# Performance work log

Hardware: AMD Instinct MI355X
Metric: run time of the kernel (lower is better)

The kernel has to match this reference:

```python
import jax, jax.numpy as jnp
import numpy as np

B, NPG, DIN, ED, DEG = 16, 1024, 16, 8, 32
HEADS, OUT1 = 5, 6
HID = HEADS * OUT1          # 30 features after conv1
C1, C2 = 32, 4              # DIFFPool cluster counts
N = B * NPG                 # 16384 total nodes
E = N * DEG                 # 524288 edges


def _egat_conv(x, src, dst, eattr, W, a_s, a_d, We, heads, outc, n_nodes):
    # Edge-gated GAT: per-edge attention logits from src/dst node features plus
    # a linear projection of edge attributes, segment-softmax over incoming edges.
    h = (x @ W).reshape(n_nodes, heads, outc)
    logit = jax.nn.leaky_relu((h[src] * a_s).sum(-1) + (h[dst] * a_d).sum(-1) + eattr @ We, 0.2)  # [E, heads]
    m = jax.ops.segment_max(logit, dst, num_segments=n_nodes)
    ex = jnp.exp(logit - m[dst])
    den = jax.ops.segment_sum(ex, dst, num_segments=n_nodes)
    alpha = ex / (den[dst] + 1e-16)
    out = jax.ops.segment_sum(alpha[:, :, None] * h[src], dst, num_segments=n_nodes)
    return out.reshape(n_nodes, heads * outc), alpha


def _diff_pool(x, adj, s_logits, b, n, c, d):
    s = jax.nn.softmax(s_logits.reshape(b, n, c), axis=-1)
    xp = jnp.einsum('bnc,bnd->bcd', s, x.reshape(b, n, d))
    adjp = jnp.einsum('bnc,bnm,bmk->bck', s, adj, s)
    reg = jnp.mean((adj - jnp.einsum('bnc,bmc->bnm', s, s)) ** 2)  # link-pred loss
    return xp.reshape(b * c, d), adjp, reg


def _dense_edges(b, c):
    base = jnp.arange(c)
    off = (jnp.arange(b) * c)[:, None]
    src = (jnp.repeat(base, c)[None, :] + off).reshape(-1)
    dst = (jnp.tile(base, c)[None, :] + off).reshape(-1)
    return src, dst


def _forward(x, edge_index, edge_attr, adj, params):
    (W1, a_src1, a_dst1, We1, Wp1, as_p1, ad_p1, Wep1,
     Wp2, as_p2, ad_p2, Wep2, Wf1, bf1, Wf2, bf2) = params
    src, dst = edge_index[0], edge_index[1]
    x1, e = _egat_conv(x, src, dst, edge_attr, W1, a_src1, a_dst1, We1, HEADS, OUT1, N)  # [N,30]
    e_dot = jnp.prod(e, axis=-1)[:, None]  # _EGATConv.dot: product over heads (unused downstream)
    s1, _ = _egat_conv(x1, src, dst, edge_attr, Wp1, as_p1, ad_p1, Wep1, 1, C1, N)
    x2, adj2, reg1 = _diff_pool(x1, adj, s1, B, NPG, C1, HID)
    src2, dst2 = _dense_edges(B, C1)
    ea2 = adj2.reshape(B * C1 * C1, 1)  # pooled graph is dense; adj values as edge attrs
    s2, _ = _egat_conv(x2, src2, dst2, ea2, Wp2, as_p2, ad_p2, Wep2, 1, C2, B * C1)
    x3, _, reg2 = _diff_pool(x2, adj2, s2, B, C1, C2, HID)
    reg = reg1 * 10.0 + reg2 * 0.1
    z = x3.reshape(B, C2 * HID)
    z = jax.nn.relu(z @ Wf1 + bf1)
    logits = z @ Wf2 + bf2
    return logits, reg


def setup_inputs() -> dict:
    key = jax.random.key(0)
    ks = jax.random.split(key, 20)
    # block-diagonal random edges: each graph has NPG*DEG edges within its block
    src_l = jax.random.randint(ks[0], (B, NPG * DEG), 0, NPG)
    dst_l = jax.random.randint(ks[1], (B, NPG * DEG), 0, NPG)
    off = (jnp.arange(B) * NPG)[:, None]
    edge_index = jnp.stack([(src_l + off).reshape(-1), (dst_l + off).reshape(-1)])
    adj = jnp.zeros((B, NPG, NPG), jnp.float32).at[jnp.arange(B)[:, None], src_l, dst_l].set(1.0)
    edge_attr = jax.random.uniform(ks[2], (E, ED), jnp.float32)
    x = jax.random.normal(ks[3], (N, DIN), jnp.float32)
    y = jax.random.randint(ks[4], (B,), 0, 2)

    def nrm(k, shape, fan):
        return jax.random.normal(k, shape, jnp.float32) / np.float32(np.sqrt(fan))

    return dict(
        x=x, edge_index=edge_index, edge_attr=edge_attr, y=y, adj=adj,
        W1=nrm(ks[5], (DIN, HEADS * OUT1), DIN),
        a_src1=nrm(ks[6], (HEADS, OUT1), OUT1),
        a_dst1=nrm(ks[7], (HEADS, OUT1), OUT1),
        We1=nrm(ks[8], (ED, HEADS), ED),
        Wp1=nrm(ks[9], (HID, C1), HID),
        as_p1=nrm(ks[10], (1, C1), C1),
        ad_p1=nrm(ks[11], (1, C1), C1),
        Wep1=nrm(ks[12], (ED, 1), ED),
        Wp2=nrm(ks[13], (HID, C2), HID),
        as_p2=nrm(ks[14], (1, C2), C2),
        ad_p2=nrm(ks[15], (1, C2), C2),
        Wep2=nrm(ks[16], (1, 1), 1),
        Wf1=nrm(ks[17], (C2 * HID, 32), C2 * HID),
        bf1=jnp.zeros((32,), jnp.float32),
        Wf2=nrm(ks[18], (32, 2), 32),
        bf2=jnp.zeros((2,), jnp.float32),
    )


def reference(x, edge_index, edge_attr, y, adj, W1, a_src1, a_dst1, We1, Wp1, as_p1, ad_p1, Wep1, Wp2, as_p2, ad_p2, Wep2, Wf1, bf1, Wf2, bf2):
    params = (W1, a_src1, a_dst1, We1, Wp1, as_p1, ad_p1, Wep1,
              Wp2, as_p2, ad_p2, Wep2, Wf1, bf1, Wf2, bf2)
    return _forward(x, edge_index, edge_attr, adj, params)
```

## Files before the change

kernel.cpp:

```cpp
#include <hip/hip_runtime.h>
#include <math.h>

#define NB 16
#define NPG 1024
#define DIN 16
#define ED 8
#define NHEADS 5
#define OUT1 6
#define HID 30
#define C1 32
#define C2 4
#define NN (NB*NPG)
#define EE (NN*32)
#define EPG 32768
#define CH 16
#define CE 2048

__device__ __forceinline__ float lrelu(float v){ return v >= 0.f ? v : 0.2f*v; }

__device__ __forceinline__ void chunk_gc(int& g, int& c){
    int x = blockIdx.x & 7;
    int j = blockIdx.x >> 3;
    g = x + 8*(j >> 4);
    c = j & 15;
}

__device__ __forceinline__ size_t xcd_chunk_base(){
    int x = blockIdx.x & 7;
    int j = blockIdx.x >> 3;
    int g = x + 8*(j >> 7);
    int c = j & 127;
    return (size_t)g*EPG + (size_t)c*256;
}

__global__ void k_hist_chunk(const int* __restrict__ src, const int* __restrict__ dst,
                             int* __restrict__ histD, int* __restrict__ histS,
                             const float* __restrict__ x, const float* __restrict__ W1,
                             const float* __restrict__ as1, const float* __restrict__ ad1,
                             float* __restrict__ h1, float* __restrict__ hs1, float* __restrict__ hd1){
    int t = threadIdx.x;
    if (blockIdx.x < 256){
        __shared__ int hD[NPG], hS[NPG];
        for (int i = t; i < NPG; i += 256){ hD[i] = 0; hS[i] = 0; }
        __syncthreads();
        int g, c; chunk_gc(g, c);
        size_t e0 = ((size_t)g*CH + c)*CE;
        #pragma unroll
        for (int i = 0; i < 8; i++){
            size_t e = e0 + i*256 + t;
            atomicAdd(&hD[dst[e] & (NPG-1)], 1);
            atomicAdd(&hS[src[e] & (NPG-1)], 1);
        }
        __syncthreads();
        size_t hb = ((size_t)g*CH + c)*NPG;
        for (int i = t; i < NPG; i += 256){
            histD[hb + i] = hD[i];
            histS[hb + i] = hS[i];
        }
        return;
    }
    __shared__ float Ws[DIN*HID];
    __shared__ float as_s[HID], ad_s[HID];
    for (int i = t; i < DIN*HID; i += blockDim.x) Ws[i] = W1[i];
    if (t < HID){ as_s[t] = as1[t]; ad_s[t] = ad1[t]; }
    __syncthreads();
    int n = (blockIdx.x - 256)*blockDim.x + t;
    if (n >= NN) return;
    float xv[DIN];
    #pragma unroll
    for (int i = 0; i < DIN; i++) xv[i] = x[n*DIN + i];
    float hv[HID];
    #pragma unroll
    for (int j = 0; j < HID; j++){
        float a = 0.f;
        #pragma unroll
        for (int i = 0; i < DIN; i++) a += xv[i]*Ws[i*HID + j];
        hv[j] = a; h1[(size_t)n*HID + j] = a;
    }
    #pragma unroll
    for (int h = 0; h < NHEADS; h++){
        float s = 0.f, d = 0.f;
        #pragma unroll
        for (int c2 = 0; c2 < OUT1; c2++){ s += hv[h*OUT1+c2]*as_s[h*OUT1+c2]; d += hv[h*OUT1+c2]*ad_s[h*OUT1+c2]; }
        hs1[n*NHEADS + h] = s; hd1[n*NHEADS + h] = d;
    }
}

__global__ __launch_bounds__(1024) void k_cumscan(int* __restrict__ histD, int* __restrict__ histS,
                                                  int* __restrict__ rowptr, int* __restrict__ rowptrS){
    __shared__ int wtot[16], wbase[16];
    bool isD = (blockIdx.x < NB);
    int b = isD ? blockIdx.x : (blockIdx.x - NB);
    int* hist = isD ? histD : histS;
    int* rp   = isD ? rowptr : rowptrS;
    int n = threadIdx.x;
    int run = 0;
    #pragma unroll
    for (int c = 0; c < CH; c++){
        size_t idx = ((size_t)b*CH + c)*NPG + n;
        int v = hist[idx];
        hist[idx] = run;
        run += v;
    }
    int lane = n & 63, wv = n >> 6;
    int sincl = run;
    #pragma unroll
    for (int off = 1; off < 64; off <<= 1){
        int v = __shfl_up(sincl, off, 64);
        if (lane >= off) sincl += v;
    }
    if (lane == 63) wtot[wv] = sincl;
    __syncthreads();
    if (n == 0){
        int r = 0;
        #pragma unroll
        for (int w = 0; w < 16; w++){ wbase[w] = r; r += wtot[w]; }
    }
    __syncthreads();
    int excl = wbase[wv] + sincl - run;
    rp[b*NPG + n] = b*EPG + excl;
    if (b == NB-1 && n == NPG-1) rp[NN] = EE;
}

__global__ void k_scatter_det(const int* __restrict__ src, const int* __restrict__ dst,
                              const int* __restrict__ rowptr, const int* __restrict__ rowptrS,
                              const int* __restrict__ histD, const int* __restrict__ histS,
                              int* __restrict__ srcs, int* __restrict__ eid,
                              int* __restrict__ dsts, int* __restrict__ nbrS){
    __shared__ int baseD[NPG], baseS[NPG];
    int t = threadIdx.x;
    int g, c; chunk_gc(g, c);
    size_t hb = ((size_t)g*CH + c)*NPG;
    for (int i = t; i < NPG; i += 256){
        baseD[i] = rowptr[g*NPG + i] + histD[hb + i];
        baseS[i] = rowptrS[g*NPG + i] + histS[hb + i];
    }
    __syncthreads();
    size_t e0 = ((size_t)g*CH + c)*CE;
    #pragma unroll
    for (int i = 0; i < 8; i++){
        size_t e = e0 + i*256 + t;
        int s = src[e], d = dst[e];
        int p = atomicAdd(&baseD[d & (NPG-1)], 1);
        srcs[p] = s; eid[p] = (int)e; dsts[p] = d;
        int pS = atomicAdd(&baseS[s & (NPG-1)], 1);
        nbrS[pS] = d;
    }
}

__global__ void k_elogit(const float* __restrict__ ea, const float* __restrict__ We1,
                         const float* __restrict__ Wep1,
                         const int* __restrict__ srcs, const int* __restrict__ eid,
                         const int* __restrict__ dsts,
                         const float* __restrict__ hs1, const float* __restrict__ hd1,
                         float* __restrict__ lg1T, float* __restrict__ ewp1s){
    __shared__ float W[ED*NHEADS];
    __shared__ float Wp[ED];
    int t = threadIdx.x;
    if (t < ED*NHEADS) W[t] = We1[t];
    if (t < ED) Wp[t] = Wep1[t];
    __syncthreads();
    size_t k = xcd_chunk_base() + t;
    int s = srcs[k], e = eid[k], d = dsts[k];
    float a[ED];
    #pragma unroll
    for (int i = 0; i < ED; i++) a[i] = ea[(size_t)e*ED + i];
    const float* hsr = hs1 + (size_t)s*NHEADS;
    const float* hdr = hd1 + (size_t)d*NHEADS;
    #pragma unroll
    for (int h = 0; h < NHEADS; h++){
        float sv = 0.f;
        #pragma unroll
        for (int i = 0; i < ED; i++) sv += a[i]*W[i*NHEADS + h];
        lg1T[(size_t)h*EE + k] = lrelu(hsr[h] + hdr[h] + sv);
    }
    float sv = 0.f;
    #pragma unroll
    for (int i = 0; i < ED; i++) sv += a[i]*Wp[i];
    ewp1s[k] = sv;
}

__global__ __launch_bounds__(640) void k_conv1_agg(const int* __restrict__ srcs,
                            const int* __restrict__ rowptr,
                            const float* __restrict__ h1, const float* __restrict__ lg1T,
                            float* __restrict__ x1){
    __shared__ float hls[NPG*HID];
    int t = threadIdx.x;
    int xx = blockIdx.x & 7;
    int j = blockIdx.x >> 3;
    int g = xx + 8*(j >> 4);
    int seg = j & 15;
    const float* hg = h1 + (size_t)g*NPG*HID;
    for (int i = t; i < NPG*HID; i += 640) hls[i] = hg[i];
    __syncthreads();
    int nl = seg*64 + t/10;
    int r = t - (t/10)*10;
    int h = r >> 1;
    int q = r & 1;
    int n = g*NPG + nl;
    int k0 = rowptr[n], k1 = rowptr[n+1];
    const float* lgh = lg1T + (size_t)h*EE;
    int off = h*OUT1 + q*3;
    float m = -INFINITY, den = 0.f;
    float acc[3] = {0.f, 0.f, 0.f};
    int k = k0;
    for (; k + 4 <= k1; k += 4){
        float l0 = lgh[k+0], l1 = lgh[k+1], l2 = lgh[k+2], l3 = lgh[k+3];
        int s0 = srcs[k+0] & (NPG-1), s1 = srcs[k+1] & (NPG-1);
        int s2 = srcs[k+2] & (NPG-1), s3 = srcs[k+3] & (NPG-1);
        const float* p0 = hls + s0*HID + off;
        const float* p1 = hls + s1*HID + off;
        const float* p2 = hls + s2*HID + off;
        const float* p3 = hls + s3*HID + off;
        float mb = fmaxf(fmaxf(l0, l1), fmaxf(l2, l3));
        float mn = fmaxf(m, mb);
        float f  = expf(m - mn);
        float e0 = expf(l0 - mn), e1 = expf(l1 - mn);
        float e2 = expf(l2 - mn), e3 = expf(l3 - mn);
        m = mn;
        den = den*f + e0 + e1 + e2 + e3;
        #pragma unroll
        for (int c = 0; c < 3; c++)
            acc[c] = acc[c]*f + e0*p0[c] + e1*p1[c] + e2*p2[c] + e3*p3[c];
    }
    for (; k < k1; k++){
        float l = lgh[k];
        int s = srcs[k] & (NPG-1);
        float mn = fmaxf(m, l);
        float f  = expf(m - mn);
        float ex = expf(l - mn);
        m = mn;
        den = den*f + ex;
        const float* hr = hls + s*HID + off;
        #pragma unroll
        for (int c = 0; c < 3; c++) acc[c] = acc[c]*f + ex*hr[c];
    }
    float inv = 1.f / (den + 1e-16f);
    #pragma unroll
    for (int c = 0; c < 3; c++) x1[(size_t)n*HID + off + c] = acc[c]*inv;
}

__global__ void k_pd(const float* __restrict__ x1, const float* __restrict__ Wp1,
                     const float* __restrict__ asp, const float* __restrict__ adp,
                     float* __restrict__ hp1, float* __restrict__ hsp, float* __restrict__ hdp,
                     const int* __restrict__ rowptrS, const int* __restrict__ nbrS,
                     int* __restrict__ unbr, int* __restrict__ ucnt,
                     float* __restrict__ scal){
    __shared__ float Ws[HID*C1];
    __shared__ float as_s[C1], ad_s[C1];
    __shared__ unsigned int bm[256*33];
    __shared__ int red[256];
    int t = threadIdx.x;
    if (blockIdx.x < 64){
        for (int i = t; i < HID*C1; i += blockDim.x) Ws[i] = Wp1[i];
        if (t < C1){ as_s[t] = asp[t]; ad_s[t] = adp[t]; }
        __syncthreads();
        int n = blockIdx.x*blockDim.x + t;
        float xv[HID];
        #pragma unroll
        for (int d = 0; d < HID; d++) xv[d] = x1[(size_t)n*HID + d];
        float s = 0.f, dd = 0.f;
        for (int c = 0; c < C1; c++){
            float a = 0.f;
            #pragma unroll
            for (int d = 0; d < HID; d++) a += xv[d]*Ws[d*C1 + c];
            hp1[(size_t)n*C1 + c] = a;
            s += a*as_s[c]; dd += a*ad_s[c];
        }
        hsp[n] = s; hdp[n] = dd;
        return;
    }
    unsigned int* mybm = &bm[t*33];
    #pragma unroll
    for (int i = 0; i < 32; i++) mybm[i] = 0u;
    int n = (blockIdx.x - 64)*blockDim.x + t;
    int cnt = 0;
    {
        int k0 = rowptrS[n], k1 = rowptrS[n+1];
        for (int k = k0; k < k1; k++){
            int m = nbrS[k];
            int loc = m & (NPG-1);
            unsigned int w = (unsigned int)(loc >> 5);
            unsigned int bit = 1u << (loc & 31);
            unsigned int old = mybm[w];
            if (!(old & bit)){
                mybm[w] = old | bit;
                unbr[k0 + cnt] = m;
                cnt++;
            }
        }
        ucnt[n] = cnt;
    }
    red[t] = cnt; __syncthreads();
    for (int s = 128; s > 0; s >>= 1){ if (t < s) red[t] += red[t+s]; __syncthreads(); }
    if (t == 0) atomicAdd(&scal[0], (float)red[0]);
}

__global__ __launch_bounds__(512) void k_pool1_agg(const int* __restrict__ srcs,
                            const int* __restrict__ rowptr,
                            const float* __restrict__ hp1, const float* __restrict__ hsp,
                            const float* __restrict__ hdp, const float* __restrict__ ewp1s,
                            float* __restrict__ ssoft){
    __shared__ float hls[NPG*33];
    __shared__ float sm[64*33];
    __shared__ float hsps[NPG];
    __shared__ float hdps[64];
    int t = threadIdx.x;
    int xx = blockIdx.x & 7;
    int j = blockIdx.x >> 3;
    int g = xx + 8*(j >> 4);
    int seg = j & 15;
    const float* hg = hp1 + (size_t)g*NPG*C1;
    for (int i = t; i < NPG*C1; i += 512){
        int s = i >> 5, c = i & 31;
        hls[s*33 + c] = hg[i];
    }
    for (int i = t; i < NPG; i += 512) hsps[i] = hsp[g*NPG + i];
    if (t < 64) hdps[t] = hdp[g*NPG + seg*64 + t];
    __syncthreads();
    int nl = t >> 3, q = t & 7;
    int n = g*NPG + seg*64 + nl;
    int k0 = rowptr[n], k1 = rowptr[n+1];
    float hdv = hdps[nl];
    float m = -INFINITY, den = 0.f;
    float acc[4] = {0.f, 0.f, 0.f, 0.f};
    int k = k0;
    for (; k + 4 <= k1; k += 4){
        int sl0 = srcs[k+0] & (NPG-1), sl1 = srcs[k+1] & (NPG-1);
        int sl2 = srcs[k+2] & (NPG-1), sl3 = srcs[k+3] & (NPG-1);
        float l0 = lrelu(hsps[sl0] + hdv + ewp1s[k+0]);
        float l1 = lrelu(hsps[sl1] + hdv + ewp1s[k+1]);
        float l2 = lrelu(hsps[sl2] + hdv + ewp1s[k+2]);
        float l3 = lrelu(hsps[sl3] + hdv + ewp1s[k+3]);
        int b0 = sl0*33 + q*4, b1 = sl1*33 + q*4;
        int b2 = sl2*33 + q*4, b3 = sl3*33 + q*4;
        float mb = fmaxf(fmaxf(l0, l1), fmaxf(l2, l3));
        float mn = fmaxf(m, mb);
        float f  = expf(m - mn);
        float e0 = expf(l0 - mn), e1 = expf(l1 - mn);
        float e2 = expf(l2 - mn), e3 = expf(l3 - mn);
        m = mn;
        den = den*f + e0 + e1 + e2 + e3;
        #pragma unroll
        for (int c = 0; c < 4; c++)
            acc[c] = acc[c]*f + e0*hls[b0+c] + e1*hls[b1+c] + e2*hls[b2+c] + e3*hls[b3+c];
    }
    for (; k < k1; k++){
        int sl = srcs[k] & (NPG-1);
        float l = lrelu(hsps[sl] + hdv + ewp1s[k]);
        int b = sl*33 + q*4;
        float mn = fmaxf(m, l);
        float f  = expf(m - mn);
        float ex = expf(l - mn);
        m = mn;
        den = den*f + ex;
        #pragma unroll
        for (int c = 0; c < 4; c++) acc[c] = acc[c]*f + ex*hls[b+c];
    }
    float inv = 1.f / (den + 1e-16f);
    #pragma unroll
    for (int c = 0; c < 4; c++) sm[nl*33 + q*4 + c] = acc[c]*inv;
    __syncthreads();
    float mx = -INFINITY;
    #pragma unroll 8
    for (int i = 0; i < C1; i++) mx = fmaxf(mx, sm[nl*33 + i]);
    float sum = 0.f;
    #pragma unroll 8
    for (int i = 0; i < C1; i++) sum += expf(sm[nl*33 + i] - mx);
    float is = 1.f/sum;
    #pragma unroll
    for (int c = 0; c < 4; c++)
        ssoft[(size_t)n*C1 + q*4 + c] = expf(sm[nl*33 + q*4 + c] - mx)*is;
}

__global__ __launch_bounds__(512) void k_T(const int* __restrict__ rowptrS,
                    const int* __restrict__ unbr,
                    const int* __restrict__ ucnt, const float* __restrict__ ssoft,
                    float* __restrict__ T){
    __shared__ float sls[NPG*33];
    int t = threadIdx.x;
    int xx = blockIdx.x & 7;
    int j = blockIdx.x >> 3;
    int g = xx + 8*(j >> 4);
    int seg = j & 15;
    const float* sg = ssoft + (size_t)g*NPG*C1;
    for (int i = t; i < NPG*C1; i += 512){
        int s = i >> 5, c = i & 31;
        sls[s*33 + c] = sg[i];
    }
    __syncthreads();
    int nl = t >> 3, q = t & 7;
    int n = g*NPG + seg*64 + nl;
    int k0 = rowptrS[n];
    int cnt = ucnt[n];
    float acc[4] = {0.f, 0.f, 0.f, 0.f};
    int i = 0;
    for (; i + 4 <= cnt; i += 4){
        int b0 = (unbr[k0+i+0] & (NPG-1))*33 + q*4;
        int b1 = (unbr[k0+i+1] & (NPG-1))*33 + q*4;
        int b2 = (unbr[k0+i+2] & (NPG-1))*33 + q*4;
        int b3 = (unbr[k0+i+3] & (NPG-1))*33 + q*4;
        #pragma unroll
        for (int c = 0; c < 4; c++)
            acc[c] += sls[b0+c] + sls[b1+c] + sls[b2+c] + sls[b3+c];
    }
    for (; i < cnt; i++){
        int b = (unbr[k0+i] & (NPG-1))*33 + q*4;
        #pragma unroll
        for (int c = 0; c < 4; c++) acc[c] += sls[b+c];
    }
    #pragma unroll
    for (int c = 0; c < 4; c++) T[(size_t)n*C1 + q*4 + c] = acc[c];
}

__global__ void k_partials(const float* __restrict__ ssoft, const float* __restrict__ T,
                           const float* __restrict__ x1,
                           float* __restrict__ adj2, float* __restrict__ Gm,
                           float* __restrict__ x2){
    int b  = blockIdx.y;
    int n0 = blockIdx.x * 64;
    int t  = threadIdx.x;
    __shared__ float ssh[64*C1];
    __shared__ float tsh[64*C1];
    __shared__ float xsh[64*HID];
    {
        size_t sbase = ((size_t)b*NPG + n0)*C1;
        #pragma unroll
        for (int i = 0; i < 8; i++){
            int lin = t + i*256;
            ssh[lin] = ssoft[sbase + lin];
            tsh[lin] = T[sbase + lin];
        }
        size_t xbase = ((size_t)b*NPG + n0)*HID;
        for (int lin = t; lin < 64*HID; lin += 256) xsh[lin] = x1[xbase + lin];
    }
    __syncthreads();
    float accA[4] = {0,0,0,0}, accG[4] = {0,0,0,0}, accX[4] = {0,0,0,0};
    int cA[4], kA[4], cX[4], dX[4];
    #pragma unroll
    for (int q = 0; q < 4; q++){
        int p = t + q*256;
        cA[q] = p >> 5; kA[q] = p & 31;
        cX[q] = p / HID; dX[q] = p - cX[q]*HID;
    }
    for (int r = 0; r < 64; r++){
        const float* sr = ssh + r*C1;
        const float* tr = tsh + r*C1;
        const float* xr = xsh + r*HID;
        #pragma unroll
        for (int q = 0; q < 4; q++){
            float sc = sr[cA[q]];
            accA[q] += sc*tr[kA[q]];
            accG[q] += sc*sr[kA[q]];
        }
        #pragma unroll
        for (int q = 0; q < 4; q++){
            int p = t + q*256;
            if (p < C1*HID) accX[q] += sr[cX[q]]*xr[dX[q]];
        }
    }
    #pragma unroll
    for (int q = 0; q < 4; q++){
        int p = t + q*256;
        atomicAdd(&adj2[(size_t)b*1024 + p], accA[q]);
        atomicAdd(&Gm[(size_t)b*1024 + p], accG[q]);
        if (p < C1*HID) atomicAdd(&x2[((size_t)b*C1 + cX[q])*HID + dX[q]], accX[q]);
    }
}

__global__ __launch_bounds__(256) void k_tail(const float* __restrict__ x2, const float* __restrict__ adj2,
                       const float* __restrict__ Gm,
                       const float* __restrict__ Wp2, const float* __restrict__ asp,
                       const float* __restrict__ adp, const float* __restrict__ Wep2,
                       const float* __restrict__ Wf1, const float* __restrict__ bf1,
                       const float* __restrict__ Wf2, const float* __restrict__ bf2,
                       float* __restrict__ out, float* __restrict__ scal,
                       unsigned int* __restrict__ ctr){
    int b = blockIdx.x;
    int t = threadIdx.x;
    __shared__ float x2s[C1*HID];
    __shared__ float a2s[C1*C1];
    __shared__ float Wps[HID*C2];
    __shared__ float Wf1s[C2*HID*32];
    __shared__ float asps[C2], adps[C2];
    __shared__ float bf1s[32], Wf2s[64], bf2s[2];
    __shared__ float wepsh;
    __shared__ float h2s[C1*C2];
    __shared__ float hs2s[C1], hd2s[C1];
    __shared__ float sss[C1*C2];
    __shared__ float x3s[C2*HID];
    __shared__ float zsh[32];
    __shared__ float red[256], red2[256];

    float gv[4];
    #pragma unroll
    for (int q = 0; q < 4; q++) gv[q] = Gm[(size_t)b*1024 + t + q*256];
    for (int i = t; i < C1*HID; i += 256) x2s[i] = x2[(size_t)b*C1*HID + i];
    for (int i = t; i < C1*C1; i += 256) a2s[i] = adj2[(size_t)b*C1*C1 + i];
    for (int i = t; i < C2*HID*32; i += 256) Wf1s[i] = Wf1[i];
    if (t < HID*C2) Wps[t] = Wp2[t];
    if (t < C2){ asps[t] = asp[t]; adps[t] = adp[t]; }
    if (t < 32) bf1s[t] = bf1[t];
    if (t < 64) Wf2s[t] = Wf2[t];
    if (t < 2)  bf2s[t] = bf2[t];
    if (t == 0) wepsh = Wep2[0];
    __syncthreads();

    if (t < C1*C2){
        int i = t >> 2, c = t & 3;
        float a = 0.f;
        #pragma unroll
        for (int d = 0; d < HID; d++) a += x2s[i*HID + d]*Wps[d*C2 + c];
        h2s[t] = a;
    }
    {
        float lfr = gv[0]*gv[0] + gv[1]*gv[1] + gv[2]*gv[2] + gv[3]*gv[3];
        float ltr = (t < C1) ? a2s[t*33] : 0.f;
        red[t] = ltr; red2[t] = lfr;
        __syncthreads();
        for (int s = 128; s > 0; s >>= 1){
            if (t < s){ red[t] += red[t+s]; red2[t] += red2[t+s]; }
            __syncthreads();
        }
        if (t == 0){ atomicAdd(&scal[1], red[0]); atomicAdd(&scal[2], red2[0]); }
    }
    if (t < C1){
        float s = 0.f, dd = 0.f;
        #pragma unroll
        for (int c = 0; c < C2; c++){ s += h2s[t*C2 + c]*asps[c]; dd += h2s[t*C2 + c]*adps[c]; }
        hs2s[t] = s; hd2s[t] = dd;
    }
    __syncthreads();
    if (t < C1){
        int j = t;
        float hdv = hd2s[j];
        float wep = wepsh;
        float m = -INFINITY;
        for (int i = 0; i < C1; i++)
            m = fmaxf(m, lrelu(hs2s[i] + hdv + a2s[i*C1 + j]*wep));
        float den = 0.f;
        float acc[C2] = {0,0,0,0};
        for (int i = 0; i < C1; i++){
            float ex = expf(lrelu(hs2s[i] + hdv + a2s[i*C1 + j]*wep) - m);
            den += ex;
            #pragma unroll
            for (int c = 0; c < C2; c++) acc[c] += ex * h2s[i*C2 + c];
        }
        float inv = 1.f/(den + 1e-16f);
        float v[C2]; float mx = -INFINITY;
        #pragma unroll
        for (int c = 0; c < C2; c++){ v[c] = acc[c]*inv; mx = fmaxf(mx, v[c]); }
        float sum = 0.f;
        #pragma unroll
        for (int c = 0; c < C2; c++){ v[c] = expf(v[c] - mx); sum += v[c]; }
        float i2 = 1.f/sum;
        #pragma unroll
        for (int c = 0; c < C2; c++) sss[j*C2 + c] = v[c]*i2;
    }
    __syncthreads();
    if (t < C2*HID){
        int c = t / HID, d = t % HID;
        float a = 0.f;
        #pragma unroll
        for (int n = 0; n < C1; n++) a += sss[n*C2 + c]*x2s[n*HID + d];
        x3s[t] = a;
    }
    {
        float loc = 0.f;
        for (int p = t; p < 1024; p += 256){
            int n = p >> 5, mm = p & 31;
            float dot = 0.f;
            #pragma unroll
            for (int c = 0; c < C2; c++) dot += sss[n*C2 + c]*sss[mm*C2 + c];
            float df = a2s[p] - dot;
            loc += df*df;
        }
        red[t] = loc; __syncthreads();
        for (int s = 128; s > 0; s >>= 1){ if (t < s) red[t] += red[t+s]; __syncthreads(); }
        if (t == 0) atomicAdd(&scal[3], red[0]);
        __syncthreads();
    }
    if (t < 32){
        float a = bf1s[t];
        #pragma unroll 8
        for (int k = 0; k < C2*HID; k++) a += x3s[k]*Wf1s[k*32 + t];
        zsh[t] = fmaxf(a, 0.f);
    }
    __syncthreads();
    if (t < 2){
        float a = bf2s[t];
        #pragma unroll
        for (int j = 0; j < 32; j++) a += zsh[j]*Wf2s[j*2 + t];
        out[b*2 + t] = a;
    }
    if (t == 0){
        __threadfence();
        unsigned int old = atomicAdd(ctr, 1u);
        if (old == NB - 1){
            float adjsum = atomicAdd(&scal[0], 0.f);
            float tr     = atomicAdd(&scal[1], 0.f);
            float fr     = atomicAdd(&scal[2], 0.f);
            float r2     = atomicAdd(&scal[3], 0.f);
            float reg1 = (adjsum - 2.f*tr + fr) * (1.f/16777216.f);
            float reg2 = r2 * (1.f/16384.f);
            out[32] = 10.f*reg1 + 0.1f*reg2;
        }
    }
}

extern "C" void kernel_launch(void* const* d_in, const int* in_sizes, int n_in,
                              void* d_out, int out_size, void* d_ws, size_t ws_size,
                              hipStream_t stream) {
    const float* x    = (const float*)d_in[0];
    const int*   ei   = (const int*)d_in[1];
    const float* ea   = (const float*)d_in[2];
    const float* W1   = (const float*)d_in[5];
    const float* as1  = (const float*)d_in[6];
    const float* ad1  = (const float*)d_in[7];
    const float* We1  = (const float*)d_in[8];
    const float* Wp1  = (const float*)d_in[9];
    const float* asp1 = (const float*)d_in[10];
    const float* adp1 = (const float*)d_in[11];
    const float* Wep1 = (const float*)d_in[12];
    const float* Wp2  = (const float*)d_in[13];
    const float* asp2 = (const float*)d_in[14];
    const float* adp2 = (const float*)d_in[15];
    const float* Wep2 = (const float*)d_in[16];
    const float* Wf1  = (const float*)d_in[17];
    const float* bf1  = (const float*)d_in[18];
    const float* Wf2  = (const float*)d_in[19];
    const float* bf2  = (const float*)d_in[20];
    float* out = (float*)d_out;

    const int* srcA = ei;
    const int* dstA = ei + EE;

    char* wp = (char*)d_ws;
    auto carve = [&](size_t bytes)->char*{
        char* p = wp;
        wp += (bytes + 255) & ~(size_t)255;
        return p;
    };
    float* h1    = (float*)carve((size_t)NN*HID*4);
    float* hs1   = (float*)carve((size_t)NN*NHEADS*4);
    float* hd1   = (float*)carve((size_t)NN*NHEADS*4);
    float* lg1T  = (float*)carve((size_t)EE*NHEADS*4);
    float* ewp1s = (float*)carve((size_t)EE*4);
    float* x1    = (float*)carve((size_t)NN*HID*4);
    float* hp1   = (float*)carve((size_t)NN*C1*4);
    float* hsp   = (float*)carve((size_t)NN*4);
    float* hdp   = (float*)carve((size_t)NN*4);
    float* ssoft = (float*)carve((size_t)NN*C1*4);
    float* T     = (float*)carve((size_t)NN*C1*4);
    float* x2    = (float*)carve((size_t)NB*C1*HID*4);
    float* adj2  = (float*)carve((size_t)NB*C1*C1*4);
    float* Gm    = (float*)carve((size_t)NB*C1*C1*4);
    float* scal  = (float*)carve(16*4);
    unsigned int* ctr = (unsigned int*)(scal + 8);
    int* histD   = (int*)carve((size_t)NB*CH*NPG*4);
    int* histS   = (int*)carve((size_t)NB*CH*NPG*4);
    int* rowptr  = (int*)carve((size_t)(NN+1)*4);
    int* rowptrS = (int*)carve((size_t)(NN+1)*4);
    int* srcs    = (int*)carve((size_t)EE*4);
    int* eid     = (int*)carve((size_t)EE*4);
    int* dsts    = (int*)carve((size_t)EE*4);
    int* nbrS    = (int*)carve((size_t)EE*4);
    int* unbr    = (int*)carve((size_t)EE*4);
    int* ucnt    = (int*)carve((size_t)NN*4);

    hipMemsetAsync(scal, 0, 16*4, stream);
    hipMemsetAsync(x2, 0, (size_t)(NB*C1*HID + 2*NB*C1*C1)*4, stream);

    const int TB = 256;

    k_hist_chunk<<<dim3(256 + 64), TB, 0, stream>>>(srcA, dstA, histD, histS,
                                                    x, W1, as1, ad1, h1, hs1, hd1);
    k_cumscan<<<dim3(2*NB), 1024, 0, stream>>>(histD, histS, rowptr, rowptrS);
    k_scatter_det<<<dim3(256), TB, 0, stream>>>(srcA, dstA, rowptr, rowptrS,
                                                histD, histS, srcs, eid, dsts, nbrS);

    k_elogit<<<dim3(2048), TB, 0, stream>>>(ea, We1, Wep1, srcs, eid, dsts, hs1, hd1, lg1T, ewp1s);

    k_conv1_agg<<<dim3(256), 640, 0, stream>>>(srcs, rowptr, h1, lg1T, x1);

    k_pd<<<dim3(128), TB, 0, stream>>>(x1, Wp1, asp1, adp1, hp1, hsp, hdp,
                                       rowptrS, nbrS, unbr, ucnt, scal);

    k_pool1_agg<<<dim3(256), 512, 0, stream>>>(srcs, rowptr, hp1, hsp, hdp, ewp1s, ssoft);

    k_T<<<dim3(256), 512, 0, stream>>>(rowptrS, unbr, ucnt, ssoft, T);
    k_partials<<<dim3(16, NB), TB, 0, stream>>>(ssoft, T, x1, adj2, Gm, x2);

    k_tail<<<dim3(NB), TB, 0, stream>>>(x2, adj2, Gm, Wp2, asp2, adp2, Wep2,
                                        Wf1, bf1, Wf2, bf2, out, scal, ctr);
}
```

Baseline: 275.0 us.

## Fuse tail into partials via last-block counter and vectorize shared-memory staging loads

The per-graph tail kernel is merged into k_partials: each block bumps a per-graph counter after its atomics, and the last of the 16 blocks for that graph reads the accumulated Gm/x2/adj2 with atomic loads and runs the tail computation. This removes one kernel launch and its dependency gap. Global-to-shared staging loops in several kernels are also switched to float4 loads. The fusion adds a threadfence and counter atomics and serializes the tail work onto one block per graph.

```diff
diff --git a/kernel.cpp b/kernel.cpp
--- a/kernel.cpp
+++ b/kernel.cpp
@@ -18,6 +18,10 @@
 
 __device__ __forceinline__ float lrelu(float v){ return v >= 0.f ? v : 0.2f*v; }
 
+__device__ __forceinline__ float aload(const float* p){
+    return __hip_atomic_load(p, __ATOMIC_RELAXED, __HIP_MEMORY_SCOPE_AGENT);
+}
+
 __device__ __forceinline__ void chunk_gc(int& g, int& c){
     int x = blockIdx.x & 7;
     int j = blockIdx.x >> 3;
@@ -184,14 +188,15 @@
                             const int* __restrict__ rowptr,
                             const float* __restrict__ h1, const float* __restrict__ lg1T,
                             float* __restrict__ x1){
-    __shared__ float hls[NPG*HID];
+    __shared__ __align__(16) float hls[NPG*HID];
     int t = threadIdx.x;
     int xx = blockIdx.x & 7;
     int j = blockIdx.x >> 3;
     int g = xx + 8*(j >> 4);
     int seg = j & 15;
-    const float* hg = h1 + (size_t)g*NPG*HID;
-    for (int i = t; i < NPG*HID; i += 640) hls[i] = hg[i];
+    const float4* hg4 = (const float4*)(h1 + (size_t)g*NPG*HID);
+    float4* hls4 = (float4*)hls;
+    for (int i = t; i < NPG*HID/4; i += 640) hls4[i] = hg4[i];
     __syncthreads();
     int nl = seg*64 + t/10;
     int r = t - (t/10)*10;
@@ -303,19 +308,25 @@
                             float* __restrict__ ssoft){
     __shared__ float hls[NPG*33];
     __shared__ float sm[64*33];
-    __shared__ float hsps[NPG];
+    __shared__ __align__(16) float hsps[NPG];
     __shared__ float hdps[64];
     int t = threadIdx.x;
     int xx = blockIdx.x & 7;
     int j = blockIdx.x >> 3;
     int g = xx + 8*(j >> 4);
     int seg = j & 15;
-    const float* hg = hp1 + (size_t)g*NPG*C1;
-    for (int i = t; i < NPG*C1; i += 512){
-        int s = i >> 5, c = i & 31;
-        hls[s*33 + c] = hg[i];
-    }
-    for (int i = t; i < NPG; i += 512) hsps[i] = hsp[g*NPG + i];
+    const float4* hg4 = (const float4*)(hp1 + (size_t)g*NPG*C1);
+    for (int i = t; i < NPG*C1/4; i += 512){
+        float4 v = hg4[i];
+        int s = i >> 3, c = (i & 7)*4;
+        float* p = &hls[s*33 + c];
+        p[0] = v.x; p[1] = v.y; p[2] = v.z; p[3] = v.w;
+    }
+    {
+        const float4* hs4 = (const float4*)(hsp + (size_t)g*NPG);
+        float4* hsps4 = (float4*)hsps;
+        for (int i = t; i < NPG/4; i += 512) hsps4[i] = hs4[i];
+    }
     if (t < 64) hdps[t] = hdp[g*NPG + seg*64 + t];
     __syncthreads();
     int nl = t >> 3, q = t & 7;
@@ -383,10 +394,12 @@
     int j = blockIdx.x >> 3;
     int g = xx + 8*(j >> 4);
     int seg = j & 15;
-    const float* sg = ssoft + (size_t)g*NPG*C1;
-    for (int i = t; i < NPG*C1; i += 512){
-        int s = i >> 5, c = i & 31;
-        sls[s*33 + c] = sg[i];
+    const float4* sg4 = (const float4*)(ssoft + (size_t)g*NPG*C1);
+    for (int i = t; i < NPG*C1/4; i += 512){
+        float4 v = sg4[i];
+        int s = i >> 3, c = (i & 7)*4;
+        float* p = &sls[s*33 + c];
+        p[0] = v.x; p[1] = v.y; p[2] = v.z; p[3] = v.w;
     }
     __syncthreads();
     int nl = t >> 3, q = t & 7;
@@ -413,26 +426,34 @@
     for (int c = 0; c < 4; c++) T[(size_t)n*C1 + q*4 + c] = acc[c];
 }
 
-__global__ void k_partials(const float* __restrict__ ssoft, const float* __restrict__ T,
+__global__ __launch_bounds__(256) void k_partials(const float* __restrict__ ssoft, const float* __restrict__ T,
                            const float* __restrict__ x1,
                            float* __restrict__ adj2, float* __restrict__ Gm,
-                           float* __restrict__ x2){
+                           float* __restrict__ x2,
+                           const float* __restrict__ Wp2, const float* __restrict__ asp,
+                           const float* __restrict__ adp, const float* __restrict__ Wep2,
+                           const float* __restrict__ Wf1, const float* __restrict__ bf1,
+                           const float* __restrict__ Wf2, const float* __restrict__ bf2,
+                           float* __restrict__ out, float* __restrict__ scal,
+                           unsigned int* __restrict__ ctr, unsigned int* __restrict__ gctr){
     int b  = blockIdx.y;
     int n0 = blockIdx.x * 64;
     int t  = threadIdx.x;
-    __shared__ float ssh[64*C1];
-    __shared__ float tsh[64*C1];
-    __shared__ float xsh[64*HID];
+    __shared__ __align__(16) float ssh[64*C1];
+    __shared__ __align__(16) float tsh[64*C1];
+    __shared__ __align__(16) float xsh[64*HID];
     {
         size_t sbase = ((size_t)b*NPG + n0)*C1;
-        #pragma unroll
-        for (int i = 0; i < 8; i++){
-            int lin = t + i*256;
-            ssh[lin] = ssoft[sbase + lin];
-            tsh[lin] = T[sbase + lin];
-        }
+        const float4* s4 = (const float4*)(ssoft + sbase);
+        const float4* t4 = (const float4*)(T + sbase);
+        float4* ssh4 = (float4*)ssh;
+        float4* tsh4 = (float4*)tsh;
+        #pragma unroll
+        for (int i = 0; i < 2; i++){ ssh4[t + i*256] = s4[t + i*256]; tsh4[t + i*256] = t4[t + i*256]; }
         size_t xbase = ((size_t)b*NPG + n0)*HID;
-        for (int lin = t; lin < 64*HID; lin += 256) xsh[lin] = x1[xbase + lin];
+        const float4* x4 = (const float4*)(x1 + xbase);
+        float4* xsh4 = (float4*)xsh;
+        for (int i = t; i < 64*HID/4; i += 256) xsh4[i] = x4[i];
     }
     __syncthreads();
     float accA[4] = {0,0,0,0}, accG[4] = {0,0,0,0}, accX[4] = {0,0,0,0};
@@ -466,18 +487,16 @@
         atomicAdd(&Gm[(size_t)b*1024 + p], accG[q]);
         if (p < C1*HID) atomicAdd(&x2[((size_t)b*C1 + cX[q])*HID + dX[q]], accX[q]);
     }
-}
-
-__global__ __launch_bounds__(256) void k_tail(const float* __restrict__ x2, const float* __restrict__ adj2,
-                       const float* __restrict__ Gm,
-                       const float* __restrict__ Wp2, const float* __restrict__ asp,
-                       const float* __restrict__ adp, const float* __restrict__ Wep2,
-                       const float* __restrict__ Wf1, const float* __restrict__ bf1,
-                       const float* __restrict__ Wf2, const float* __restrict__ bf2,
-                       float* __restrict__ out, float* __restrict__ scal,
-                       unsigned int* __restrict__ ctr){
-    int b = blockIdx.x;
-    int t = threadIdx.x;
+
+    __threadfence();
+    __syncthreads();
+    __shared__ unsigned int lastsh;
+    if (t == 0) lastsh = atomicAdd(&gctr[b], 1u);
+    __syncthreads();
+    if (lastsh != 15u) return;
+    if (t == 0) __threadfence();
+    __syncthreads();
+
     __shared__ float x2s[C1*HID];
     __shared__ float a2s[C1*C1];
     __shared__ float Wps[HID*C2];
@@ -494,9 +513,9 @@
 
     float gv[4];
     #pragma unroll
-    for (int q = 0; q < 4; q++) gv[q] = Gm[(size_t)b*1024 + t + q*256];
-    for (int i = t; i < C1*HID; i += 256) x2s[i] = x2[(size_t)b*C1*HID + i];
-    for (int i = t; i < C1*C1; i += 256) a2s[i] = adj2[(size_t)b*C1*C1 + i];
+    for (int q = 0; q < 4; q++) gv[q] = aload(&Gm[(size_t)b*1024 + t + q*256]);
+    for (int i = t; i < C1*HID; i += 256) x2s[i] = aload(&x2[(size_t)b*C1*HID + i]);
+    for (int i = t; i < C1*C1; i += 256) a2s[i] = aload(&adj2[(size_t)b*C1*C1 + i]);
     for (int i = t; i < C2*HID*32; i += 256) Wf1s[i] = Wf1[i];
     if (t < HID*C2) Wps[t] = Wp2[t];
     if (t < C2){ asps[t] = asp[t]; adps[t] = adp[t]; }
@@ -590,7 +609,7 @@
     if (t < 2){
         float a = bf2s[t];
         #pragma unroll
-        for (int j = 0; j < 32; j++) a += zsh[j]*Wf2s[j*2 + t];
+        for (int j2 = 0; j2 < 32; j2++) a += zsh[j2]*Wf2s[j2*2 + t];
         out[b*2 + t] = a;
     }
     if (t == 0){
@@ -655,8 +674,9 @@
     float* x2    = (float*)carve((size_t)NB*C1*HID*4);
     float* adj2  = (float*)carve((size_t)NB*C1*C1*4);
     float* Gm    = (float*)carve((size_t)NB*C1*C1*4);
-    float* scal  = (float*)carve(16*4);
-    unsigned int* ctr = (unsigned int*)(scal + 8);
+    float* scal  = (float*)carve(64*4);
+    unsigned int* ctr  = (unsigned int*)(scal + 8);
+    unsigned int* gctr = (unsigned int*)(scal + 16);
     int* histD   = (int*)carve((size_t)NB*CH*NPG*4);
     int* histS   = (int*)carve((size_t)NB*CH*NPG*4);
     int* rowptr  = (int*)carve((size_t)(NN+1)*4);
@@ -668,7 +688,7 @@
     int* unbr    = (int*)carve((size_t)EE*4);
     int* ucnt    = (int*)carve((size_t)NN*4);
 
-    hipMemsetAsync(scal, 0, 16*4, stream);
+    hipMemsetAsync(scal, 0, 64*4, stream);
     hipMemsetAsync(x2, 0, (size_t)(NB*C1*HID + 2*NB*C1*C1)*4, stream);
 
     const int TB = 256;
@@ -689,8 +709,8 @@
     k_pool1_agg<<<dim3(256), 512, 0, stream>>>(srcs, rowptr, hp1, hsp, hdp, ewp1s, ssoft);
 
     k_T<<<dim3(256), 512, 0, stream>>>(rowptrS, unbr, ucnt, ssoft, T);
-    k_partials<<<dim3(16, NB), TB, 0, stream>>>(ssoft, T, x1, adj2, Gm, x2);
-
-    k_tail<<<dim3(NB), TB, 0, stream>>>(x2, adj2, Gm, Wp2, asp2, adp2, Wep2,
-                                        Wf1, bf1, Wf2, bf2, out, scal, ctr);
-}
+
+    k_partials<<<dim3(16, NB), TB, 0, stream>>>(ssoft, T, x1, adj2, Gm, x2,
+                                                Wp2, asp2, adp2, Wep2,
+                                                Wf1, bf1, Wf2, bf2, out, scal, ctr, gctr);
+}
```

Result: slower. 288.2 us (+4.8%).
